# Kernel tuning notes

Hardware: AMD Instinct MI355X
Metric: run time of the kernel (lower is better)

The kernel has to match this reference:

```python
import jax, jax.numpy as jnp
import numpy as np

EPS = 1e-12
FP8_MAX = 448.0  # torch.finfo(float8_e4m3fn).max
G = 128  # tile/block group size


def per_tile_quant_dequant(x):
    # x: [seq, din]; one scale per 1x128 tile along din (per_tile_quant semantics)
    s, d = x.shape
    xt = x.reshape(s, d // G, G)
    amax = jnp.max(jnp.abs(xt), axis=-1, keepdims=True)
    scale = jnp.maximum(amax, EPS) / FP8_MAX
    q = jnp.clip(xt / scale, -FP8_MAX, FP8_MAX).astype(jnp.float8_e4m3fn)
    return (q.astype(jnp.float32) * scale).reshape(s, d)


def per_block_quant_dequant(w):
    # w: [ne, dout, din]; one scale per 128x128 block
    ne, dout, din = w.shape
    wb = w.reshape(ne, dout // G, G, din // G, G)
    amax = jnp.max(jnp.abs(wb), axis=(2, 4), keepdims=True)
    scale = jnp.maximum(amax, EPS) / FP8_MAX
    q = jnp.clip(wb / scale, -FP8_MAX, FP8_MAX).astype(jnp.float8_e4m3fn)
    return (q.astype(jnp.float32) * scale).reshape(ne, dout, din)


def grouped_gemm(xq, wq, tokens_per_expert):
    # xq: [seq, din] (tokens contiguous per expert); wq: [ne, dout, din]
    seq = xq.shape[0]
    ne, dout, _ = wq.shape
    ends = jnp.cumsum(tokens_per_expert)
    starts = ends - tokens_per_expert
    tok = jnp.arange(seq)
    out = jnp.zeros((seq, dout), dtype=jnp.float32)
    for e in range(ne):  # small fixed expert count
        mask = ((tok >= starts[e]) & (tok < ends[e]))[:, None]
        xe = jnp.where(mask, xq, 0.0)
        out = out + xe @ wq[e].T
    return out


def setup_inputs() -> dict:
    key = jax.random.key(0)
    k1, k2 = jax.random.split(key)
    ne, dout, din, seq = 8, 2048, 2048, 8192
    x = jax.random.normal(k1, (seq, din), dtype=jnp.float32)
    # weight stored flat as (ne*dout, din), as in the module
    weight = jax.random.normal(k2, (ne * dout, din), dtype=jnp.float32) * 0.02
    tokens_per_expert = jnp.full((ne,), seq // ne, dtype=jnp.int32)
    return {"input": x, "weight": weight, "tokens_per_expert": tokens_per_expert}


def reference(input, weight, tokens_per_expert):
    ne, dout, din = 8, 2048, 2048
    w = weight.reshape(ne, dout, din)
    xq = per_tile_quant_dequant(input)          # per-tile fp8 activation quant
    wq = per_block_quant_dequant(w)             # per-block fp8 weight quant
    return grouped_gemm(xq, wq, tokens_per_expert)
```

## Files before the change

kernel.cpp:

```cpp
#include <hip/hip_runtime.h>
#include <hip/hip_bf16.h>
#include <stdint.h>

#define NE   8
#define DOUT 2048
#define DIN  2048
#define SEQ  8192
#define GSZ  128
#define FP8_MAX 448.0f
#define EPSQ 1e-12f

typedef float f32x4 __attribute__((ext_vector_type(4)));

__device__ __forceinline__ void async16(void* lds_base, const void* gptr) {
    __builtin_amdgcn_global_load_lds(
        (const __attribute__((address_space(1))) unsigned int*)gptr,
        (__attribute__((address_space(3))) unsigned int*)lds_base,
        16, 0, 0);
}

__global__ __launch_bounds__(256) void quant_x_kernel(
    const float* __restrict__ x, unsigned char* __restrict__ qx,
    float* __restrict__ sx)
{
    const int g = blockIdx.x * 256 + threadIdx.x;
    const float4 v = ((const float4*)x)[g];
    float a = fmaxf(fmaxf(fabsf(v.x), fabsf(v.y)),
                    fmaxf(fabsf(v.z), fabsf(v.w)));
    #pragma unroll
    for (int o = 16; o; o >>= 1) a = fmaxf(a, __shfl_xor(a, o));
    const float scale = fmaxf(a, EPSQ) / FP8_MAX;
    const int tile = g >> 5;
    if ((threadIdx.x & 31) == 0) sx[tile] = scale;

    float q0 = fminf(fmaxf(v.x / scale, -FP8_MAX), FP8_MAX);
    float q1 = fminf(fmaxf(v.y / scale, -FP8_MAX), FP8_MAX);
    float q2 = fminf(fmaxf(v.z / scale, -FP8_MAX), FP8_MAX);
    float q3 = fminf(fmaxf(v.w / scale, -FP8_MAX), FP8_MAX);
    int lo = __builtin_amdgcn_cvt_pk_fp8_f32(q0, q1, 0, false);
    int pk = __builtin_amdgcn_cvt_pk_fp8_f32(q2, q3, lo, true);
    ((unsigned int*)qx)[g] = (unsigned int)pk;
}

__global__ __launch_bounds__(256) void quant_w_kernel(
    const float* __restrict__ w, unsigned char* __restrict__ qw,
    float* __restrict__ sw)
{
    __shared__ float buf[128 * 128];
    __shared__ float red[4];

    const int cb = blockIdx.x;
    const int rb = blockIdx.y;
    const int e  = blockIdx.z;
    const int t  = threadIdx.x;
    const int lane = t & 63, wv = t >> 6;

    const size_t base = ((size_t)e * DOUT + rb * GSZ) * DIN + cb * GSZ;
    const float* wp = w + base;

    #pragma unroll
    for (int j = 0; j < 16; ++j) {
        int f16 = (wv * 16 + j) * 64 + lane;
        int row = f16 >> 5, cc = f16 & 31;
        async16(buf + (wv * 16 + j) * 256,
                wp + (size_t)row * DIN + cc * 4);
    }
    __syncthreads();

    float a = 0.f;
    #pragma unroll
    for (int i = 0; i < 16; ++i) {
        f32x4 v = *(const f32x4*)(buf + (t + i * 256) * 4);
        a = fmaxf(a, fmaxf(fmaxf(fabsf(v[0]), fabsf(v[1])),
                           fmaxf(fabsf(v[2]), fabsf(v[3]))));
    }
    #pragma unroll
    for (int o = 32; o; o >>= 1) a = fmaxf(a, __shfl_xor(a, o));
    if (lane == 0) red[wv] = a;
    __syncthreads();
    a = fmaxf(fmaxf(red[0], red[1]), fmaxf(red[2], red[3]));
    const float scale = fmaxf(a, EPSQ) / FP8_MAX;
    if (t == 0) sw[(e * 16 + rb) * 16 + cb] = scale;

    unsigned int* qout = (unsigned int*)(qw + base);
    #pragma unroll
    for (int i = 0; i < 16; ++i) {
        int idx = t + i * 256;
        f32x4 v = *(const f32x4*)(buf + idx * 4);
        float q0 = fminf(fmaxf(v[0] / scale, -FP8_MAX), FP8_MAX);
        float q1 = fminf(fmaxf(v[1] / scale, -FP8_MAX), FP8_MAX);
        float q2 = fminf(fmaxf(v[2] / scale, -FP8_MAX), FP8_MAX);
        float q3 = fminf(fmaxf(v[3] / scale, -FP8_MAX), FP8_MAX);
        int lo = __builtin_amdgcn_cvt_pk_fp8_f32(q0, q1, 0, false);
        int pk = __builtin_amdgcn_cvt_pk_fp8_f32(q2, q3, lo, true);
        int r = idx >> 5, c4 = idx & 31;
        qout[r * (DIN / 4) + c4] = (unsigned int)pk;
    }
}

__global__ __launch_bounds__(256, 3) void gemm_kernel(
    const unsigned char* __restrict__ qx, const float* __restrict__ sx,
    const unsigned char* __restrict__ qw, const float* __restrict__ sw,
    const int* __restrict__ tpe, float* __restrict__ out)
{
    __shared__ unsigned char Asm[128 * 128];
    __shared__ unsigned char Bsm[128 * 128];
    __shared__ float sxT[16 * 128];

    const int tid  = threadIdx.x;
    const int lane = tid & 63;
    const int wv   = tid >> 6;
    const int wm   = wv >> 1, wn = wv & 1;
    const int quad = lane >> 4;
    const int l16  = lane & 15;
    const int nb   = blockIdx.x;
    const int mb   = blockIdx.y;
    const int r0   = mb * 128, n0 = nb * 128;

    int e = -1, start = 0;
    #pragma unroll
    for (int i = 0; i < NE; ++i) {
        int end = start + tpe[i];
        if (r0 >= start && r0 < end) e = i;
        start = end;
    }
    if (e < 0) {
        f32x4 z = {0.f, 0.f, 0.f, 0.f};
        for (int i = tid; i < 128 * 32; i += 256) {
            int r = i >> 5, c4 = i & 31;
            *(f32x4*)(out + (size_t)(r0 + r) * DOUT + n0 + c4 * 4) = z;
        }
        return;
    }

    {
        const float* sp = sx + (size_t)r0 * 16;
        for (int i = tid; i < 2048; i += 256) {
            int r = i >> 4, kb = i & 15;
            sxT[kb * 128 + r] = sp[i];
        }
    }

    const unsigned char* Ag = qx + (size_t)r0 * DIN;
    const unsigned char* Bg = qw + (size_t)e * DOUT * DIN + (size_t)n0 * DIN;
    const float* swp = sw + (e * 16 + nb) * 16;

    int srow[4], scol[4];
    #pragma unroll
    for (int j = 0; j < 4; ++j) {
        int f = wv * 4096 + j * 1024 + lane * 16;
        int row = f >> 7, pc = (f >> 4) & 7;
        srow[j] = row;
        scol[j] = (pc ^ (row & 7)) * 16;
    }

    int aoff[4][4];
    int boff[4][4];
    #pragma unroll
    for (int i = 0; i < 4; ++i)
        #pragma unroll
        for (int ks = 0; ks < 4; ++ks) {
            int lc = ks * 2 + (quad >> 1), wd = (quad & 1) * 8;
            int mrow = wm * 64 + i * 16 + l16;
            aoff[i][ks] = mrow * 128 + ((lc ^ (mrow & 7)) * 16) + wd;
            int nrow = wn * 64 + i * 16 + l16;
            boff[i][ks] = nrow * 128 + ((lc ^ (nrow & 7)) * 16) + wd;
        }

    f32x4 acc[4][4];
    f32x4 zero4 = {0.f, 0.f, 0.f, 0.f};
    #pragma unroll
    for (int mi = 0; mi < 4; ++mi)
        #pragma unroll
        for (int ni = 0; ni < 4; ++ni) acc[mi][ni] = zero4;

    for (int kb = 0; kb < 16; ++kb) {
        __syncthreads();
        #pragma unroll
        for (int j = 0; j < 4; ++j) {
            async16(Asm + wv * 4096 + j * 1024,
                    Ag + (size_t)srow[j] * DIN + kb * GSZ + scol[j]);
            async16(Bsm + wv * 4096 + j * 1024,
                    Bg + (size_t)srow[j] * DIN + kb * GSZ + scol[j]);
        }
        __syncthreads();

        const float swv = swp[kb];

        long bf[4][4];
        #pragma unroll
        for (int ks = 0; ks < 4; ++ks)
            #pragma unroll
            for (int ni = 0; ni < 4; ++ni)
                bf[ks][ni] = *(const long*)(Bsm + boff[ni][ks]);

        #pragma unroll
        for (int mi = 0; mi < 4; ++mi) {
            long af[4];
            #pragma unroll
            for (int ks = 0; ks < 4; ++ks)
                af[ks] = *(const long*)(Asm + aoff[mi][ks]);

            f32x4 ak[4];
            #pragma unroll
            for (int ni = 0; ni < 4; ++ni) ak[ni] = zero4;
            #pragma unroll
            for (int ks = 0; ks < 4; ++ks)
                #pragma unroll
                for (int ni = 0; ni < 4; ++ni)
                    ak[ni] = __builtin_amdgcn_mfma_f32_16x16x32_fp8_fp8(
                        af[ks], bf[ks][ni], ak[ni], 0, 0, 0);

            const f32x4 sv = *(const f32x4*)(sxT + kb * 128 + wm * 64 + mi * 16 + quad * 4);
            float s0 = sv[0] * swv, s1 = sv[1] * swv,
                  s2 = sv[2] * swv, s3 = sv[3] * swv;
            #pragma unroll
            for (int ni = 0; ni < 4; ++ni) {
                acc[mi][ni][0] += ak[ni][0] * s0;
                acc[mi][ni][1] += ak[ni][1] * s1;
                acc[mi][ni][2] += ak[ni][2] * s2;
                acc[mi][ni][3] += ak[ni][3] * s3;
            }
        }
    }

    #pragma unroll
    for (int mi = 0; mi < 4; ++mi) {
        int rbase = r0 + wm * 64 + mi * 16 + quad * 4;
        #pragma unroll
        for (int ni = 0; ni < 4; ++ni) {
            int col = n0 + wn * 64 + ni * 16 + l16;
            #pragma unroll
            for (int r = 0; r < 4; ++r)
                out[(size_t)(rbase + r) * DOUT + col] = acc[mi][ni][r];
        }
    }
}

extern "C" void kernel_launch(void* const* d_in, const int* in_sizes, int n_in,
                              void* d_out, int out_size, void* d_ws, size_t ws_size,
                              hipStream_t stream) {
    const float* x   = (const float*)d_in[0];
    const float* wt  = (const float*)d_in[1];
    const int*   tpe = (const int*)d_in[2];
    float* out = (float*)d_out;

    char* ws = (char*)d_ws;
    unsigned char* qx = (unsigned char*)ws;
    unsigned char* qw = qx + (size_t)SEQ * DIN;
    float* sx = (float*)(qw + (size_t)NE * DOUT * DIN);
    float* sw = sx + (size_t)SEQ * 16;

    quant_x_kernel<<<SEQ * DIN / 4 / 256, 256, 0, stream>>>(x, qx, sx);
    quant_w_kernel<<<dim3(16, 16, NE), 256, 0, stream>>>(wt, qw, sw);
    gemm_kernel<<<dim3(DOUT / 128, SEQ / 128), 256, 0, stream>>>(
        qx, sx, qw, sw, tpe, out);
}
```

Baseline: 320.4 us.

## Rescale accumulators by scale ratios instead of per-block temp accumulation

Replaces the per-k-block temporary MFMA accumulator plus scaled add with direct accumulation into the main accumulators. Before each k-block the accumulators are multiplied by the ratio of the previous to the current combined scale, and the final scale is applied at store. This frees the temporary registers and the per-block FMA work, which allows occupancy to rise from 3 to 4 waves per SIMD, and the LDS fragment loads are regrouped per k-step. Precomputing the ratios relies on division by scales, which can add rounding error or produce inf/NaN if a scale ratio is extreme.

```diff
diff --git a/kernel.cpp b/kernel.cpp
--- a/kernel.cpp
+++ b/kernel.cpp
@@ -98,14 +98,14 @@
     }
 }
 
-__global__ __launch_bounds__(256, 3) void gemm_kernel(
+__global__ __launch_bounds__(256, 4) void gemm_kernel(
     const unsigned char* __restrict__ qx, const float* __restrict__ sx,
     const unsigned char* __restrict__ qw, const float* __restrict__ sw,
     const int* __restrict__ tpe, float* __restrict__ out)
 {
     __shared__ unsigned char Asm[128 * 128];
     __shared__ unsigned char Bsm[128 * 128];
-    __shared__ float sxT[16 * 128];
+    __shared__ float Rs[16 * 128];
 
     const int tid  = threadIdx.x;
     const int lane = tid & 63;
@@ -134,16 +134,28 @@
     }
 
     {
-        const float* sp = sx + (size_t)r0 * 16;
+        float* Cs = (float*)Asm;
+        const float* sp  = sx + (size_t)r0 * 16;
+        const float* swp = sw + (e * 16 + nb) * 16;
         for (int i = tid; i < 2048; i += 256) {
             int r = i >> 4, kb = i & 15;
-            sxT[kb * 128 + r] = sp[i];
-        }
+            Cs[kb * 128 + r] = sp[i] * swp[kb];
+        }
+        __syncthreads();
+        float rv[8];
+        #pragma unroll
+        for (int j = 0; j < 8; ++j) {
+            int i = tid + j * 256;
+            int kb = i >> 7, row = i & 127;
+            rv[j] = (kb == 0) ? Cs[15 * 128 + row]
+                              : Cs[(kb - 1) * 128 + row] / Cs[kb * 128 + row];
+        }
+        #pragma unroll
+        for (int j = 0; j < 8; ++j) Rs[tid + j * 256] = rv[j];
     }
 
     const unsigned char* Ag = qx + (size_t)r0 * DIN;
     const unsigned char* Bg = qw + (size_t)e * DOUT * DIN + (size_t)n0 * DIN;
-    const float* swp = sw + (e * 16 + nb) * 16;
 
     int srow[4], scol[4];
     #pragma unroll
@@ -154,18 +166,17 @@
         scol[j] = (pc ^ (row & 7)) * 16;
     }
 
-    int aoff[4][4];
-    int boff[4][4];
-    #pragma unroll
-    for (int i = 0; i < 4; ++i)
-        #pragma unroll
-        for (int ks = 0; ks < 4; ++ks) {
-            int lc = ks * 2 + (quad >> 1), wd = (quad & 1) * 8;
-            int mrow = wm * 64 + i * 16 + l16;
-            aoff[i][ks] = mrow * 128 + ((lc ^ (mrow & 7)) * 16) + wd;
-            int nrow = wn * 64 + i * 16 + l16;
-            boff[i][ks] = nrow * 128 + ((lc ^ (nrow & 7)) * 16) + wd;
-        }
+    int abase[4], axr[4], bbase[4], bxr[4];
+    const int q2h = quad >> 1, wd = (quad & 1) * 8;
+    #pragma unroll
+    for (int i = 0; i < 4; ++i) {
+        int mrow = wm * 64 + i * 16 + l16;
+        abase[i] = mrow * 128 + wd + 16 * (q2h ^ (mrow & 1));
+        axr[i]   = (mrow & 7) >> 1;
+        int nrow = wn * 64 + i * 16 + l16;
+        bbase[i] = nrow * 128 + wd + 16 * (q2h ^ (nrow & 1));
+        bxr[i]   = (nrow & 7) >> 1;
+    }
 
     f32x4 acc[4][4];
     f32x4 zero4 = {0.f, 0.f, 0.f, 0.f};
@@ -185,54 +196,47 @@
         }
         __syncthreads();
 
-        const float swv = swp[kb];
-
-        long bf[4][4];
-        #pragma unroll
-        for (int ks = 0; ks < 4; ++ks)
-            #pragma unroll
-            for (int ni = 0; ni < 4; ++ni)
-                bf[ks][ni] = *(const long*)(Bsm + boff[ni][ks]);
-
-        #pragma unroll
-        for (int mi = 0; mi < 4; ++mi) {
-            long af[4];
-            #pragma unroll
-            for (int ks = 0; ks < 4; ++ks)
-                af[ks] = *(const long*)(Asm + aoff[mi][ks]);
-
-            f32x4 ak[4];
-            #pragma unroll
-            for (int ni = 0; ni < 4; ++ni) ak[ni] = zero4;
-            #pragma unroll
-            for (int ks = 0; ks < 4; ++ks)
+        if (kb) {
+            #pragma unroll
+            for (int mi = 0; mi < 4; ++mi) {
+                const f32x4 rr = *(const f32x4*)(Rs + kb * 128 + wm * 64 + mi * 16 + quad * 4);
+                #pragma unroll
+                for (int ni = 0; ni < 4; ++ni) {
+                    acc[mi][ni][0] *= rr[0];
+                    acc[mi][ni][1] *= rr[1];
+                    acc[mi][ni][2] *= rr[2];
+                    acc[mi][ni][3] *= rr[3];
+                }
+            }
+        }
+
+        #pragma unroll
+        for (int ks = 0; ks < 4; ++ks) {
+            long af[4], bf[4];
+            #pragma unroll
+            for (int i = 0; i < 4; ++i) {
+                af[i] = *(const long*)(Asm + abase[i] + 32 * (ks ^ axr[i]));
+                bf[i] = *(const long*)(Bsm + bbase[i] + 32 * (ks ^ bxr[i]));
+            }
+            #pragma unroll
+            for (int mi = 0; mi < 4; ++mi)
                 #pragma unroll
                 for (int ni = 0; ni < 4; ++ni)
-                    ak[ni] = __builtin_amdgcn_mfma_f32_16x16x32_fp8_fp8(
-                        af[ks], bf[ks][ni], ak[ni], 0, 0, 0);
-
-            const f32x4 sv = *(const f32x4*)(sxT + kb * 128 + wm * 64 + mi * 16 + quad * 4);
-            float s0 = sv[0] * swv, s1 = sv[1] * swv,
-                  s2 = sv[2] * swv, s3 = sv[3] * swv;
-            #pragma unroll
-            for (int ni = 0; ni < 4; ++ni) {
-                acc[mi][ni][0] += ak[ni][0] * s0;
-                acc[mi][ni][1] += ak[ni][1] * s1;
-                acc[mi][ni][2] += ak[ni][2] * s2;
-                acc[mi][ni][3] += ak[ni][3] * s3;
-            }
+                    acc[mi][ni] = __builtin_amdgcn_mfma_f32_16x16x32_fp8_fp8(
+                        af[mi], bf[ni], acc[mi][ni], 0, 0, 0);
         }
     }
 
     #pragma unroll
     for (int mi = 0; mi < 4; ++mi) {
+        const f32x4 fv = *(const f32x4*)(Rs + wm * 64 + mi * 16 + quad * 4);
         int rbase = r0 + wm * 64 + mi * 16 + quad * 4;
         #pragma unroll
         for (int ni = 0; ni < 4; ++ni) {
             int col = n0 + wn * 64 + ni * 16 + l16;
             #pragma unroll
             for (int r = 0; r < 4; ++r)
-                out[(size_t)(rbase + r) * DOUT + col] = acc[mi][ni][r];
+                out[(size_t)(rbase + r) * DOUT + col] = acc[mi][ni][r] * fv[r];
         }
     }
 }
```

Result: faster. 302.1 us (-5.7%).
